# Optimization experiments

Measured on AMD Instinct MI355X. Metric: run time of the kernel, lower is better.

Reference implementation:

```python
import jax, jax.numpy as jnp
import numpy as np

N_NODES = 50000
N_EDGES = 800000


def _glorot(key, shape):
    fan_in, fan_out = shape
    lim = float(np.sqrt(6.0 / (fan_in + fan_out)))
    return jax.random.uniform(key, shape, jnp.float32, -lim, lim)


def setup_inputs() -> dict:
    key = jax.random.key(0)
    ks = jax.random.split(key, 8)
    x = jax.random.normal(ks[0], (N_NODES, 2), jnp.float32)
    edge_index = jax.random.randint(ks[1], (2, N_EDGES), 0, N_NODES, jnp.int64)
    edge_weight = jax.random.uniform(ks[2], (N_EDGES,), jnp.float32)
    return {
        "x": x,
        "edge_index": edge_index,
        "edge_weight": edge_weight,
        "W1": _glorot(ks[3], (2, 128)),
        "b1": jnp.zeros((128,), jnp.float32),
        "W2": _glorot(ks[4], (128, 64)),
        "b2": jnp.zeros((64,), jnp.float32),
        "W3": _glorot(ks[5], (64, 1)),
        "b3": jnp.zeros((1,), jnp.float32),
    }


def _gcn_conv(x, W, b, src, dst, ew, n_nodes):
    # PyG GCNConv with normalize=False: out[i] = sum_{e:(j->i)} ew[e] * (x_j @ W) + b
    h = x @ W                       # [N, F_out] tiny GEMM
    msg = h[src] * ew[:, None]      # [E, F_out] gather + scale
    out = jax.ops.segment_sum(msg, dst, num_segments=n_nodes)  # scatter-add
    return out + b


def reference(x, edge_index, edge_weight, W1, b1, W2, b2, W3, b3):
    src, dst = edge_index[0], edge_index[1]  # source_to_target flow: aggregate at dst
    n = x.shape[0]
    h1 = jax.nn.relu(_gcn_conv(x, W1, b1, src, dst, edge_weight, n))
    # dropout is a no-op in eval mode
    h2 = jax.nn.relu(_gcn_conv(h1, W2, b2, src, dst, edge_weight, n))
    h3 = _gcn_conv(h2, W3, b3, src, dst, edge_weight, n)  # [N, 1]
    return h3.squeeze(-1)  # [N]
```

## Files before the change

### kernel.cpp

```cpp
#include <hip/hip_runtime.h>
#include <hip/hip_fp16.h>

#define N_NODES 50000
#define N_EDGES 800000
#define BSHIFT 8
#define NBKT ((N_NODES + 255) >> BSHIFT)
#define CAP 8192
#define P1_EDGES 4096
#define P1_BLOCKS ((N_EDGES + P1_EDGES - 1) / P1_EDGES)
#define BIN_THREADS 1024
#define SORT_THREADS 512
#define SORT_LDS_CAP 6144

__global__ void bin_edges(const int* __restrict__ src, const int* __restrict__ dst,
                          const float* __restrict__ ew, int* __restrict__ bcur,
                          unsigned* __restrict__ bpk, unsigned char* __restrict__ bdl) {
    __shared__ unsigned spk[P1_EDGES];
    __shared__ unsigned short sdst[P1_EDGES];
    __shared__ int cnt[NBKT];
    __shared__ int cbase[NBKT];
    int t = threadIdx.x;
    if (t < NBKT) cnt[t] = 0;
    __syncthreads();
    int e0 = blockIdx.x * P1_EDGES;
    for (int k = 0; k < P1_EDGES / BIN_THREADS; k++) {
        int i = k * BIN_THREADS + t;
        int e = e0 + i;
        if (e < N_EDGES) {
            int d = dst[e];
            unsigned hw = (unsigned)__half_as_ushort(__float2half(ew[e]));
            spk[i] = (unsigned)src[e] | (hw << 16);
            sdst[i] = (unsigned short)d;
            atomicAdd(&cnt[d >> BSHIFT], 1);
        }
    }
    __syncthreads();
    if (t < NBKT) {
        int v = cnt[t];
        int base = v ? atomicAdd(&bcur[t], v) : 0;
        cbase[t] = t * CAP + base;
        cnt[t] = 0;
    }
    __syncthreads();
    int nmax = N_EDGES - e0;
    if (nmax > P1_EDGES) nmax = P1_EDGES;
    for (int k = 0; k < P1_EDGES / BIN_THREADS; k++) {
        int i = k * BIN_THREADS + t;
        if (i < nmax) {
            int d = sdst[i];
            int b = d >> BSHIFT;
            int pos = cbase[b] + atomicAdd(&cnt[b], 1);
            bpk[pos] = spk[i];
            bdl[pos] = (unsigned char)(d & 255);
        }
    }
}

__global__ void sort_bucket(const int* __restrict__ bcur, const unsigned* __restrict__ bpk,
                            const unsigned char* __restrict__ bdl,
                            unsigned* __restrict__ sorted, int2* __restrict__ rowspan) {
    __shared__ unsigned spk[SORT_LDS_CAP];
    __shared__ unsigned short sdl[SORT_LDS_CAP];
    __shared__ int nh[256];
    __shared__ int scn[256];
    __shared__ int lcur[256];
    int b = blockIdx.x;
    int t = threadIdx.x;
    int base = b * CAP;
    int n = bcur[b];
    if (n > CAP) n = CAP;
    bool lds_path = (n <= SORT_LDS_CAP);
    if (t < 256) nh[t] = 0;
    __syncthreads();
    if (lds_path) {
        for (int e = t; e < n; e += SORT_THREADS) {
            spk[e] = bpk[base + e];
            unsigned short d = bdl[base + e];
            sdl[e] = d;
            atomicAdd(&nh[d], 1);
        }
    } else {
        for (int e = t; e < n; e += SORT_THREADS)
            atomicAdd(&nh[bdl[base + e]], 1);
    }
    __syncthreads();
    int v = 0;
    if (t < 256) { v = nh[t]; scn[t] = v; }
    __syncthreads();
    for (int off = 1; off < 256; off <<= 1) {
        int u = (t < 256 && t >= off) ? scn[t - off] : 0;
        __syncthreads();
        if (t < 256) scn[t] += u;
        __syncthreads();
    }
    if (t < 256) {
        int ex = scn[t] - v;
        int node = (b << BSHIFT) + t;
        if (node < N_NODES) rowspan[node] = make_int2(base + ex, base + ex + v);
        nh[t] = ex;
        lcur[t] = 0;
    }
    __syncthreads();
    if (lds_path) {
        for (int e = t; e < n; e += SORT_THREADS) {
            int dlow = sdl[e];
            int pos = base + nh[dlow] + atomicAdd(&lcur[dlow], 1);
            sorted[pos] = spk[e];
        }
    } else {
        for (int e = t; e < n; e += SORT_THREADS) {
            int dlow = bdl[base + e];
            int pos = base + nh[dlow] + atomicAdd(&lcur[dlow], 1);
            sorted[pos] = bpk[base + e];
        }
    }
}

__device__ __forceinline__ float edge_w(unsigned p) {
    return __half2float(__ushort_as_half((unsigned short)(p >> 16)));
}

#define L1_NODES_PER_BLOCK 32
__global__ void fused_l1(const int2* __restrict__ rowspan, const unsigned* __restrict__ sorted,
                         const float* __restrict__ x, const float* __restrict__ W1,
                         const float* __restrict__ b1, const float* __restrict__ W2,
                         __half* __restrict__ t2) {
    __shared__ float w2s[128 * 64];
    __shared__ float hls[4][8][128];
    for (int k = threadIdx.x; k < 128 * 64; k += 256) w2s[k] = W2[k];
    int wave = threadIdx.x >> 6;
    int lane = threadIdx.x & 63;
    float w1a = W1[lane],      w1b = W1[128 + lane];
    float w1c = W1[64 + lane], w1d = W1[192 + lane];
    float b1lo = b1[lane], b1hi = b1[64 + lane];
    __syncthreads();

    int sub = lane >> 4;
    int sl  = lane & 15;
    int base = blockIdx.x * L1_NODES_PER_BLOCK + wave * 8;

#pragma unroll
    for (int g = 0; g < 2; g++) {
        int gnode = base + g * 4 + sub;
        float a0 = 0.f, a1 = 0.f;
        if (gnode < N_NODES) {
            int2 sp = rowspan[gnode];
            for (int e = sp.x + sl; e < sp.y; e += 16) {
                unsigned p = sorted[e];
                float w = edge_w(p);
                float2 xv = ((const float2*)x)[p & 0xFFFF];
                a0 = fmaf(w, xv.x, a0);
                a1 = fmaf(w, xv.y, a1);
            }
        }
#pragma unroll
        for (int off = 1; off < 16; off <<= 1) {
            a0 += __shfl_xor(a0, off);
            a1 += __shfl_xor(a1, off);
        }
#pragma unroll
        for (int n = 0; n < 4; n++) {
            float an0 = __shfl(a0, 16 * n);
            float an1 = __shfl(a1, 16 * n);
            float hlo = fmaxf(fmaf(an0, w1a, fmaf(an1, w1b, b1lo)), 0.f);
            float hhi = fmaxf(fmaf(an0, w1c, fmaf(an1, w1d, b1hi)), 0.f);
            hls[wave][g * 4 + n][lane] = hlo;
            hls[wave][g * 4 + n][64 + lane] = hhi;
        }
    }
    float acc[8] = {0.f, 0.f, 0.f, 0.f, 0.f, 0.f, 0.f, 0.f};
#pragma unroll 2
    for (int k4 = 0; k4 < 32; k4++) {
        float w0 = w2s[(4 * k4 + 0) * 64 + lane];
        float w1 = w2s[(4 * k4 + 1) * 64 + lane];
        float w2 = w2s[(4 * k4 + 2) * 64 + lane];
        float w3 = w2s[(4 * k4 + 3) * 64 + lane];
#pragma unroll
        for (int n = 0; n < 8; n++) {
            float4 h = *(const float4*)&hls[wave][n][4 * k4];
            acc[n] = fmaf(h.x, w0, fmaf(h.y, w1, fmaf(h.z, w2, fmaf(h.w, w3, acc[n]))));
        }
    }
#pragma unroll
    for (int n = 0; n < 8; n++)
        if (base + n < N_NODES) t2[(base + n) * 64 + lane] = __float2half(acc[n]);
}

__global__ void gather2_dot3(const int2* __restrict__ rowspan, const unsigned* __restrict__ sorted,
                             const __half* __restrict__ t2, const float* __restrict__ b2,
                             const float* __restrict__ W3, float* __restrict__ t3) {
    int gtid = blockIdx.x * blockDim.x + threadIdx.x;
    int node = gtid >> 6;
    int lane = threadIdx.x & 63;
    if (node >= N_NODES) return;
    int eg  = lane >> 3;
    int fli = lane & 7;
    int2 sp = rowspan[node];
    float a0 = 0.f, a1 = 0.f, a2 = 0.f, a3 = 0.f, a4 = 0.f, a5 = 0.f, a6 = 0.f, a7 = 0.f;
    int e = sp.x + eg;
    for (; e + 8 < sp.y; e += 16) {
        unsigned p0 = sorted[e];
        unsigned p1 = sorted[e + 8];
        uint4 q0 = *(const uint4*)(t2 + (p0 & 0xFFFF) * 64 + fli * 8);
        uint4 q1 = *(const uint4*)(t2 + (p1 & 0xFFFF) * 64 + fli * 8);
        float w0 = edge_w(p0), w1 = edge_w(p1);
        float2 f;
        f = __half22float2(*(const __half2*)&q0.x); a0 = fmaf(w0, f.x, a0); a1 = fmaf(w0, f.y, a1);
        f = __half22float2(*(const __half2*)&q0.y); a2 = fmaf(w0, f.x, a2); a3 = fmaf(w0, f.y, a3);
        f = __half22float2(*(const __half2*)&q0.z); a4 = fmaf(w0, f.x, a4); a5 = fmaf(w0, f.y, a5);
        f = __half22float2(*(const __half2*)&q0.w); a6 = fmaf(w0, f.x, a6); a7 = fmaf(w0, f.y, a7);
        f = __half22float2(*(const __half2*)&q1.x); a0 = fmaf(w1, f.x, a0); a1 = fmaf(w1, f.y, a1);
        f = __half22float2(*(const __half2*)&q1.y); a2 = fmaf(w1, f.x, a2); a3 = fmaf(w1, f.y, a3);
        f = __half22float2(*(const __half2*)&q1.z); a4 = fmaf(w1, f.x, a4); a5 = fmaf(w1, f.y, a5);
        f = __half22float2(*(const __half2*)&q1.w); a6 = fmaf(w1, f.x, a6); a7 = fmaf(w1, f.y, a7);
    }
    if (e < sp.y) {
        unsigned p = sorted[e];
        uint4 q = *(const uint4*)(t2 + (p & 0xFFFF) * 64 + fli * 8);
        float w = edge_w(p);
        float2 f;
        f = __half22float2(*(const __half2*)&q.x); a0 = fmaf(w, f.x, a0); a1 = fmaf(w, f.y, a1);
        f = __half22float2(*(const __half2*)&q.y); a2 = fmaf(w, f.x, a2); a3 = fmaf(w, f.y, a3);
        f = __half22float2(*(const __half2*)&q.z); a4 = fmaf(w, f.x, a4); a5 = fmaf(w, f.y, a5);
        f = __half22float2(*(const __half2*)&q.w); a6 = fmaf(w, f.x, a6); a7 = fmaf(w, f.y, a7);
    }
#pragma unroll
    for (int off = 8; off < 64; off <<= 1) {
        a0 += __shfl_xor(a0, off); a1 += __shfl_xor(a1, off);
        a2 += __shfl_xor(a2, off); a3 += __shfl_xor(a3, off);
        a4 += __shfl_xor(a4, off); a5 += __shfl_xor(a5, off);
        a6 += __shfl_xor(a6, off); a7 += __shfl_xor(a7, off);
    }
    float4 bA = *(const float4*)(b2 + fli * 8);
    float4 bB = *(const float4*)(b2 + fli * 8 + 4);
    float4 wA = *(const float4*)(W3 + fli * 8);
    float4 wB = *(const float4*)(W3 + fli * 8 + 4);
    float h = fmaxf(a0 + bA.x, 0.f) * wA.x + fmaxf(a1 + bA.y, 0.f) * wA.y +
              fmaxf(a2 + bA.z, 0.f) * wA.z + fmaxf(a3 + bA.w, 0.f) * wA.w +
              fmaxf(a4 + bB.x, 0.f) * wB.x + fmaxf(a5 + bB.y, 0.f) * wB.y +
              fmaxf(a6 + bB.z, 0.f) * wB.z + fmaxf(a7 + bB.w, 0.f) * wB.w;
#pragma unroll
    for (int off = 1; off < 8; off <<= 1) h += __shfl_xor(h, off);
    if (lane == 0) t3[node] = h;
}

__global__ void gather3(const int2* __restrict__ rowspan, const unsigned* __restrict__ sorted,
                        const float* __restrict__ t3, const float* __restrict__ b3,
                        float* __restrict__ out) {
    int gtid = blockIdx.x * blockDim.x + threadIdx.x;
    int wid = gtid >> 6;
    int lane = threadIdx.x & 63;
    int sub = lane >> 4;
    int sl  = lane & 15;
    int node = wid * 4 + sub;
    if (node >= N_NODES) return;
    int2 sp = rowspan[node];
    float acc = 0.f;
    for (int e = sp.x + sl; e < sp.y; e += 16) {
        unsigned p = sorted[e];
        acc = fmaf(edge_w(p), t3[p & 0xFFFF], acc);
    }
#pragma unroll
    for (int off = 1; off < 16; off <<= 1) acc += __shfl_xor(acc, off);
    if (sl == 0) out[node] = acc + b3[0];
}

extern "C" void kernel_launch(void* const* d_in, const int* in_sizes, int n_in,
                              void* d_out, int out_size, void* d_ws, size_t ws_size,
                              hipStream_t stream) {
    const float* x  = (const float*)d_in[0];
    const int*   ei = (const int*)d_in[1];
    const float* ew = (const float*)d_in[2];
    const float* W1 = (const float*)d_in[3];
    const float* b1 = (const float*)d_in[4];
    const float* W2 = (const float*)d_in[5];
    const float* b2 = (const float*)d_in[6];
    const float* W3 = (const float*)d_in[7];
    const float* b3 = (const float*)d_in[8];
    float* out = (float*)d_out;

    const int* src = ei;
    const int* dst = ei + N_EDGES;

    char* p = (char*)d_ws;
    int*  bcur    = (int*)p;            p += NBKT * sizeof(int);
    p = (char*)(((uintptr_t)p + 15) & ~(uintptr_t)15);
    int2* rowspan = (int2*)p;           p += N_NODES * sizeof(int2);
    unsigned* bpk = (unsigned*)p;       p += (long)NBKT * CAP * sizeof(unsigned);
    unsigned char* bdl = (unsigned char*)p; p += (long)NBKT * CAP;
    p = (char*)(((uintptr_t)p + 15) & ~(uintptr_t)15);
    unsigned* sorted  = (unsigned*)p;   p += (long)NBKT * CAP * sizeof(unsigned);
    __half* t2    = (__half*)p;         p += 64L * N_NODES * sizeof(__half);
    float* t3     = (float*)p;          p += N_NODES * sizeof(float);

    hipMemsetAsync(bcur, 0, NBKT * sizeof(int), stream);

    bin_edges<<<P1_BLOCKS, BIN_THREADS, 0, stream>>>(src, dst, ew, bcur, bpk, bdl);
    sort_bucket<<<NBKT, SORT_THREADS, 0, stream>>>(bcur, bpk, bdl, sorted, rowspan);

    fused_l1<<<(N_NODES + L1_NODES_PER_BLOCK - 1) / L1_NODES_PER_BLOCK, 256, 0, stream>>>(
        rowspan, sorted, x, W1, b1, W2, t2);

    gather2_dot3<<<(N_NODES * 64 + 255) / 256, 256, 0, stream>>>(rowspan, sorted, t2, b2, W3, t3);

    gather3<<<((N_NODES + 3) / 4 * 64 + 255) / 256, 256, 0, stream>>>(rowspan, sorted, t3, b3, out);
}
```

Baseline: 161.4 us.

## Use MFMA fp16 for layer-2 GEMM and shrink sort buckets to 128 nodes

The layer-2 dense transform in fused_l1 now runs on MFMA 16x16x32 fp16 instructions, with h1 and a transposed fp16 copy of W2 staged in padded LDS, instead of scalar FMA loops over fp32 LDS. The bucketing pipeline moves to 128-node buckets with smaller capacity, fewer threads per block and an LDS-only sort path, which drops the global-memory fallback. The intent is to cut the arithmetic and LDS cost of the GEMM and to raise parallelism and occupancy in the sort. In exchange, h1 and W2 are rounded to fp16 before the multiply, and a bucket holding more than 3072 edges would now be truncated.

New measurement: 149.2 us. -7.5%, faster.

```diff
diff --git a/kernel.cpp b/kernel.cpp
--- a/kernel.cpp
+++ b/kernel.cpp
@@ -3,14 +3,14 @@
 
 #define N_NODES 50000
 #define N_EDGES 800000
-#define BSHIFT 8
-#define NBKT ((N_NODES + 255) >> BSHIFT)
-#define CAP 8192
-#define P1_EDGES 4096
+#define BSHIFT 7
+#define NBKT ((N_NODES + 127) >> BSHIFT)
+#define CAP 3072
+#define P1_EDGES 2048
 #define P1_BLOCKS ((N_EDGES + P1_EDGES - 1) / P1_EDGES)
-#define BIN_THREADS 1024
-#define SORT_THREADS 512
-#define SORT_LDS_CAP 6144
+#define BIN_THREADS 512
+#define SORT_THREADS 256
+#define SORT_LDS_CAP 3072
 
 __global__ void bin_edges(const int* __restrict__ src, const int* __restrict__ dst,
                           const float* __restrict__ ew, int* __restrict__ bcur,
@@ -51,7 +51,7 @@
             int b = d >> BSHIFT;
             int pos = cbase[b] + atomicAdd(&cnt[b], 1);
             bpk[pos] = spk[i];
-            bdl[pos] = (unsigned char)(d & 255);
+            bdl[pos] = (unsigned char)(d & 127);
         }
     }
 }
@@ -61,39 +61,33 @@
                             unsigned* __restrict__ sorted, int2* __restrict__ rowspan) {
     __shared__ unsigned spk[SORT_LDS_CAP];
     __shared__ unsigned short sdl[SORT_LDS_CAP];
-    __shared__ int nh[256];
-    __shared__ int scn[256];
-    __shared__ int lcur[256];
+    __shared__ int nh[128];
+    __shared__ int scn[128];
+    __shared__ int lcur[128];
     int b = blockIdx.x;
     int t = threadIdx.x;
     int base = b * CAP;
     int n = bcur[b];
     if (n > CAP) n = CAP;
-    bool lds_path = (n <= SORT_LDS_CAP);
-    if (t < 256) nh[t] = 0;
-    __syncthreads();
-    if (lds_path) {
-        for (int e = t; e < n; e += SORT_THREADS) {
-            spk[e] = bpk[base + e];
-            unsigned short d = bdl[base + e];
-            sdl[e] = d;
-            atomicAdd(&nh[d], 1);
-        }
-    } else {
-        for (int e = t; e < n; e += SORT_THREADS)
-            atomicAdd(&nh[bdl[base + e]], 1);
+    if (t < 128) nh[t] = 0;
+    __syncthreads();
+    for (int e = t; e < n; e += SORT_THREADS) {
+        spk[e] = bpk[base + e];
+        unsigned short d = bdl[base + e];
+        sdl[e] = d;
+        atomicAdd(&nh[d], 1);
     }
     __syncthreads();
     int v = 0;
-    if (t < 256) { v = nh[t]; scn[t] = v; }
-    __syncthreads();
-    for (int off = 1; off < 256; off <<= 1) {
-        int u = (t < 256 && t >= off) ? scn[t - off] : 0;
+    if (t < 128) { v = nh[t]; scn[t] = v; }
+    __syncthreads();
+    for (int off = 1; off < 128; off <<= 1) {
+        int u = (t < 128 && t >= off) ? scn[t - off] : 0;
         __syncthreads();
-        if (t < 256) scn[t] += u;
+        if (t < 128) scn[t] += u;
         __syncthreads();
     }
-    if (t < 256) {
+    if (t < 128) {
         int ex = scn[t] - v;
         int node = (b << BSHIFT) + t;
         if (node < N_NODES) rowspan[node] = make_int2(base + ex, base + ex + v);
@@ -101,18 +95,10 @@
         lcur[t] = 0;
     }
     __syncthreads();
-    if (lds_path) {
-        for (int e = t; e < n; e += SORT_THREADS) {
-            int dlow = sdl[e];
-            int pos = base + nh[dlow] + atomicAdd(&lcur[dlow], 1);
-            sorted[pos] = spk[e];
-        }
-    } else {
-        for (int e = t; e < n; e += SORT_THREADS) {
-            int dlow = bdl[base + e];
-            int pos = base + nh[dlow] + atomicAdd(&lcur[dlow], 1);
-            sorted[pos] = bpk[base + e];
-        }
+    for (int e = t; e < n; e += SORT_THREADS) {
+        int dlow = sdl[e];
+        int pos = base + nh[dlow] + atomicAdd(&lcur[dlow], 1);
+        sorted[pos] = spk[e];
     }
 }
 
@@ -121,19 +107,26 @@
 }
 
 #define L1_NODES_PER_BLOCK 32
+typedef _Float16 f16x8 __attribute__((ext_vector_type(8)));
+typedef float f32x4 __attribute__((ext_vector_type(4)));
+
 __global__ void fused_l1(const int2* __restrict__ rowspan, const unsigned* __restrict__ sorted,
                          const float* __restrict__ x, const float* __restrict__ W1,
                          const float* __restrict__ b1, const float* __restrict__ W2,
                          __half* __restrict__ t2) {
-    __shared__ float w2s[128 * 64];
-    __shared__ float hls[4][8][128];
-    for (int k = threadIdx.x; k < 128 * 64; k += 256) w2s[k] = W2[k];
-    int wave = threadIdx.x >> 6;
-    int lane = threadIdx.x & 63;
+    __shared__ __align__(16) __half hls[32][136];
+    __shared__ __align__(16) __half w2t[64][136];
+    int tid = threadIdx.x;
+    int wave = tid >> 6;
+    int lane = tid & 63;
+
+    for (int idx = tid; idx < 128 * 64; idx += 256) {
+        int k = idx >> 6, nn = idx & 63;
+        w2t[nn][k] = __float2half(W2[idx]);
+    }
     float w1a = W1[lane],      w1b = W1[128 + lane];
     float w1c = W1[64 + lane], w1d = W1[192 + lane];
     float b1lo = b1[lane], b1hi = b1[64 + lane];
-    __syncthreads();
 
     int sub = lane >> 4;
     int sl  = lane & 15;
@@ -164,26 +157,36 @@
             float an1 = __shfl(a1, 16 * n);
             float hlo = fmaxf(fmaf(an0, w1a, fmaf(an1, w1b, b1lo)), 0.f);
             float hhi = fmaxf(fmaf(an0, w1c, fmaf(an1, w1d, b1hi)), 0.f);
-            hls[wave][g * 4 + n][lane] = hlo;
-            hls[wave][g * 4 + n][64 + lane] = hhi;
-        }
-    }
-    float acc[8] = {0.f, 0.f, 0.f, 0.f, 0.f, 0.f, 0.f, 0.f};
-#pragma unroll 2
-    for (int k4 = 0; k4 < 32; k4++) {
-        float w0 = w2s[(4 * k4 + 0) * 64 + lane];
-        float w1 = w2s[(4 * k4 + 1) * 64 + lane];
-        float w2 = w2s[(4 * k4 + 2) * 64 + lane];
-        float w3 = w2s[(4 * k4 + 3) * 64 + lane];
-#pragma unroll
-        for (int n = 0; n < 8; n++) {
-            float4 h = *(const float4*)&hls[wave][n][4 * k4];
-            acc[n] = fmaf(h.x, w0, fmaf(h.y, w1, fmaf(h.z, w2, fmaf(h.w, w3, acc[n]))));
-        }
-    }
-#pragma unroll
-    for (int n = 0; n < 8; n++)
-        if (base + n < N_NODES) t2[(base + n) * 64 + lane] = __float2half(acc[n]);
+            int row = wave * 8 + g * 4 + n;
+            hls[row][lane] = __float2half(hlo);
+            hls[row][64 + lane] = __float2half(hhi);
+        }
+    }
+    __syncthreads();
+
+    int m0 = (wave & 1) * 16;
+    int n0 = (wave >> 1) * 32;
+    int fr = lane & 15;
+    int kb = (lane >> 4) * 8;
+    f32x4 acc0 = {0.f, 0.f, 0.f, 0.f};
+    f32x4 acc1 = {0.f, 0.f, 0.f, 0.f};
+#pragma unroll
+    for (int k0 = 0; k0 < 128; k0 += 32) {
+        f16x8 av  = *(const f16x8*)&hls[m0 + fr][k0 + kb];
+        f16x8 bv0 = *(const f16x8*)&w2t[n0 + fr][k0 + kb];
+        f16x8 bv1 = *(const f16x8*)&w2t[n0 + 16 + fr][k0 + kb];
+        acc0 = __builtin_amdgcn_mfma_f32_16x16x32_f16(av, bv0, acc0, 0, 0, 0);
+        acc1 = __builtin_amdgcn_mfma_f32_16x16x32_f16(av, bv1, acc1, 0, 0, 0);
+    }
+    int block0 = blockIdx.x * L1_NODES_PER_BLOCK;
+#pragma unroll
+    for (int r = 0; r < 4; r++) {
+        int node = block0 + m0 + (lane >> 4) * 4 + r;
+        if (node < N_NODES) {
+            t2[node * 64 + n0 + fr]      = __float2half(acc0[r]);
+            t2[node * 64 + n0 + 16 + fr] = __float2half(acc1[r]);
+        }
+    }
 }
 
 __global__ void gather2_dot3(const int2* __restrict__ rowspan, const unsigned* __restrict__ sorted,
```
